# Optimization experiments

Measured on AMD Instinct MI355X. Metric: run time of the kernel, lower is better.

## Reference

```python
import jax, jax.numpy as jnp
import numpy as np
from jax import lax

B, C, H, W = 4, 256, 64, 64
M = 8
CP = C // M  # 32 attention channels
KS = (3, 5, 7, 9)
EPS = 1e-5


def conv1x1(a, w, b):
    # a: [B,Ci,H,W], w: [Co,Ci], b: [Co]
    return jnp.einsum('bchw,oc->bohw', a, w) + b[None, :, None, None]


def _patches(a, k):
    # im2col with padding k//2, stride 1 (matches torch.nn.Unfold(k,1,k//2,1))
    pad = k // 2
    p = lax.conv_general_dilated_patches(a, (k, k), (1, 1), [(pad, pad), (pad, pad)])
    Bb, Cc = a.shape[0], a.shape[1]
    return p.reshape(Bb, Cc, k * k, a.shape[2], a.shape[3])  # [B,C',k^2,H,W]


def local_attn(km, qm, xm, k):
    # query is the center of each patch == qm itself (stride 1, pad k//2)
    kp = _patches(km, k)                                   # [B,C',k^2,H,W]
    scores = jnp.einsum('bckhw,bchw->bkhw', kp, qm)        # per-pixel k^2 logits
    attn = jax.nn.softmax(scores, axis=1)                  # softmax over window (dim=-2 in torch)
    xp = _patches(xm, k)                                   # [B,C',k^2,H,W]
    return jnp.einsum('bckhw,bkhw->bchw', xp, attn)        # [B,C',H,W]


def setup_inputs() -> dict:
    key = jax.random.key(0)
    ks = jax.random.split(key, 12)
    s_in = 1.0 / np.sqrt(C)
    s_out = 1.0 / np.sqrt(CP)
    return {
        'x': jax.random.normal(ks[0], (B, C, H, W), jnp.float32),
        'vessel': jax.random.uniform(ks[1], (B, 1, H, W), jnp.float32),
        'wk': jax.random.normal(ks[2], (CP, C), jnp.float32) * s_in,
        'bk': jnp.zeros((CP,), jnp.float32),
        'wq': jax.random.normal(ks[3], (CP, C), jnp.float32) * s_in,
        'bq': jnp.zeros((CP,), jnp.float32),
        'wx': jax.random.normal(ks[4], (CP, C), jnp.float32) * s_in,
        'bx': jnp.zeros((CP,), jnp.float32),
        'wf': jax.random.normal(ks[5], (C, CP), jnp.float32) * s_out,
        'bf': jnp.zeros((C,), jnp.float32),
        'gamma': jnp.ones((C,), jnp.float32),
        'beta': jnp.zeros((C,), jnp.float32),
    }


def reference(x, vessel, wk, bk, wq, bq, wx, bx, wf, bf, gamma, beta):
    km = conv1x1(x, wk, bk) * vessel   # key map masked by vessel
    qm = conv1x1(x, wq, bq)            # query map
    xm = conv1x1(x, wx, bx)            # value map
    pre = local_attn(km, qm, xm, KS[0])
    for k in KS[1:]:
        pre = pre + local_attn(km, qm, xm, k)
    y = conv1x1(pre, wf, bf)           # [B,C,H,W]
    # BatchNorm2d (training-mode batch stats)
    mean = y.mean(axis=(0, 2, 3), keepdims=True)
    var = y.var(axis=(0, 2, 3), keepdims=True)
    yn = (y - mean) * lax.rsqrt(var + EPS)
    return x + gamma[None, :, None, None] * yn + beta[None, :, None, None]
```

## Files before the change

### kernel.cpp

```cpp
#include <hip/hip_runtime.h>
#include <hip/hip_bf16.h>

typedef __hip_bfloat16 bf16;
typedef unsigned short u16;
typedef unsigned int u32;

typedef __bf16 bf16x8 __attribute__((ext_vector_type(8)));
typedef float f32x4 __attribute__((ext_vector_type(4)));

__device__ __forceinline__ float bf2f(bf16 v) { return __bfloat162float(v); }
__device__ __forceinline__ float us2f(u16 u) {
    union { u32 i; float f; } c; c.i = ((u32)u) << 16; return c.f;
}
__device__ __forceinline__ u16 f2u(float f) {
    union { bf16 b; u16 u; } c; c.b = __float2bfloat16(f); return c.u;
}
__device__ __forceinline__ void up8(const uint4 v, float* f) {
    f[0] = us2f((u16)(v.x & 0xffff)); f[1] = us2f((u16)(v.x >> 16));
    f[2] = us2f((u16)(v.y & 0xffff)); f[3] = us2f((u16)(v.y >> 16));
    f[4] = us2f((u16)(v.z & 0xffff)); f[5] = us2f((u16)(v.z >> 16));
    f[6] = us2f((u16)(v.w & 0xffff)); f[7] = us2f((u16)(v.w >> 16));
}

__global__ __launch_bounds__(256) void k_proj(
    const float* __restrict__ x, const float* __restrict__ vessel,
    const float* __restrict__ wk, const float* __restrict__ bk,
    const float* __restrict__ wq, const float* __restrict__ bq,
    const float* __restrict__ wx, const float* __restrict__ bx,
    bf16* __restrict__ km, bf16* __restrict__ qm, bf16* __restrict__ xm)
{
    __shared__ u16 xs[64 * 264];
    __shared__ u16 wsh[48 * 264];
    const int tid = threadIdx.x;
    const int bid = blockIdx.x;
    const int nh = bid & 1;
    const int pt = bid >> 1;
    const int b  = pt >> 6;
    const int p0 = (pt & 63) * 64;

#pragma unroll
    for (int i = 0; i < 16; ++i) {
        const int idx4 = tid + i * 256;
        const int ch = idx4 >> 4;
        const int px4 = (idx4 & 15) * 4;
        const float4 v = *(const float4*)&x[(b * 256 + ch) * 4096 + p0 + px4];
        xs[(px4 + 0) * 264 + ch] = f2u(v.x);
        xs[(px4 + 1) * 264 + ch] = f2u(v.y);
        xs[(px4 + 2) * 264 + ch] = f2u(v.z);
        xs[(px4 + 3) * 264 + ch] = f2u(v.w);
    }
#pragma unroll
    for (int i = 0; i < 12; ++i) {
        const int idx4 = tid + i * 256;
        const int o = idx4 >> 6;
        const int ch4 = (idx4 & 63) * 4;
        const int go = nh * 48 + o;
        const float* wp = (go < 32) ? wk : ((go < 64) ? wq : wx);
        const float4 v = *(const float4*)&wp[(go & 31) * 256 + ch4];
        wsh[o * 264 + ch4 + 0] = f2u(v.x);
        wsh[o * 264 + ch4 + 1] = f2u(v.y);
        wsh[o * 264 + ch4 + 2] = f2u(v.z);
        wsh[o * 264 + ch4 + 3] = f2u(v.w);
    }
    __syncthreads();

    const int w = tid >> 6;
    const int lane = tid & 63;
    const int lm = lane & 15, quad = lane >> 4;

    f32x4 acc0 = {0.f, 0.f, 0.f, 0.f};
    f32x4 acc1 = {0.f, 0.f, 0.f, 0.f};
    f32x4 acc2 = {0.f, 0.f, 0.f, 0.f};
#pragma unroll
    for (int kk = 0; kk < 8; ++kk) {
        const int k0 = kk * 32 + quad * 8;
        const bf16x8 a  = *(const bf16x8*)&xs[(w * 16 + lm) * 264 + k0];
        const bf16x8 b0 = *(const bf16x8*)&wsh[(0 + lm) * 264 + k0];
        const bf16x8 b1 = *(const bf16x8*)&wsh[(16 + lm) * 264 + k0];
        const bf16x8 b2 = *(const bf16x8*)&wsh[(32 + lm) * 264 + k0];
        acc0 = __builtin_amdgcn_mfma_f32_16x16x32_bf16(a, b0, acc0, 0, 0, 0);
        acc1 = __builtin_amdgcn_mfma_f32_16x16x32_bf16(a, b1, acc1, 0, 0, 0);
        acc2 = __builtin_amdgcn_mfma_f32_16x16x32_bf16(a, b2, acc2, 0, 0, 0);
    }
#pragma unroll
    for (int t = 0; t < 3; ++t) {
        const f32x4 acc = (t == 0) ? acc0 : ((t == 1) ? acc1 : acc2);
        const int go = nh * 48 + t * 16 + lm;
        const float* bs = (go < 32) ? bk : ((go < 64) ? bq : bx);
        const float bias = bs[go & 31];
        bf16* dst = (go < 32) ? km : ((go < 64) ? qm : xm);
#pragma unroll
        for (int rg = 0; rg < 4; ++rg) {
            const int px = p0 + w * 16 + quad * 4 + rg;
            float vv = acc[rg] + bias;
            if (go < 32) vv *= vessel[b * 4096 + px];
            dst[(b * 4096 + px) * 32 + (go & 31)] = __float2bfloat16(vv);
        }
    }
}

__global__ __launch_bounds__(256) void k_attn(
    const bf16* __restrict__ km, const bf16* __restrict__ qm,
    const bf16* __restrict__ xm, bf16* __restrict__ pre)
{
    __shared__ u16 kT[192 * 40];
    __shared__ u16 qs[32 * 40];
    __shared__ u16 xTt[32 * 200];
    __shared__ float S[32 * 196];
    u16* P = kT;

    const int tid = threadIdx.x;
    const int b = blockIdx.x >> 7;
    const int t128 = blockIdx.x & 127;
    const int h0 = (t128 >> 3) * 4;
    const int w0 = (t128 & 7) * 8;
    const u16* uk = (const u16*)km;
    const u16* ux = (const u16*)xm;
    const uint4 z4 = {0u, 0u, 0u, 0u};

#pragma unroll
    for (int i = 0; i < 3; ++i) {
        const int idx4 = tid + i * 256;
        const int pos = idx4 >> 2, c8 = idx4 & 3;
        const int gh = h0 - 4 + (pos >> 4), gw = w0 - 4 + (pos & 15);
        uint4 kv = z4, xv = z4;
        if (gh >= 0 && gh < 64 && gw >= 0 && gw < 64) {
            const int g = ((b << 12) + (gh << 6) + gw) * 32 + c8 * 8;
            kv = *(const uint4*)&uk[g];
            xv = *(const uint4*)&ux[g];
        }
        *(uint4*)&kT[pos * 40 + c8 * 8] = kv;
        const u16* xu = (const u16*)&xv;
#pragma unroll
        for (int t = 0; t < 8; ++t)
            xTt[(c8 * 8 + t) * 200 + pos] = xu[t];
    }
    if (tid < 128) {
        const int px = tid >> 2, c8 = tid & 3;
        const int gh = h0 + (px >> 3), gw = w0 + (px & 7);
        const int g = ((b << 12) + (gh << 6) + gw) * 32 + c8 * 8;
        *(uint4*)&qs[px * 40 + c8 * 8] = *(const uint4*)&((const u16*)qm)[g];
    }
    __syncthreads();

    const int w = tid >> 6;
    const int lane = tid & 63;
    const int lm = lane & 15, quad = lane >> 4;

#pragma unroll
    for (int i = 0; i < 6; ++i) {
        const int t = w + i * 4;
        const int m = t / 12, n = t - m * 12;
        const bf16x8 a = *(const bf16x8*)&qs[(m * 16 + lm) * 40 + quad * 8];
        const bf16x8 bb = *(const bf16x8*)&kT[(n * 16 + lm) * 40 + quad * 8];
        f32x4 acc = {0.f, 0.f, 0.f, 0.f};
        acc = __builtin_amdgcn_mfma_f32_16x16x32_bf16(a, bb, acc, 0, 0, 0);
#pragma unroll
        for (int rg = 0; rg < 4; ++rg)
            S[(m * 16 + quad * 4 + rg) * 196 + n * 16 + lm] = acc[rg];
    }
    __syncthreads();

    const int px = tid >> 3, cg = tid & 7;
    const int ty = px >> 3, tx = px & 7;
    float e[24];
    float Z3 = 0.f, Z5 = 0.f, Z7 = 0.f, Z9 = 0.f;
#pragma unroll
    for (int i = 0; i < 24; ++i) {
        const int pos = cg + 8 * i;
        const int hy = pos >> 4, hx = pos & 15;
        const int dy = hy - 4 - ty, dx = hx - 4 - tx;
        const int ady = dy < 0 ? -dy : dy, adx = dx < 0 ? -dx : dx;
        const int r = ady > adx ? ady : adx;
        const float s = S[px * 196 + pos];
        const float ev = (r <= 4) ? __expf(s) : 0.f;
        e[i] = ev;
        if (r <= 1) Z3 += ev;
        if (r <= 2) Z5 += ev;
        if (r <= 3) Z7 += ev;
        Z9 += ev;
    }
#pragma unroll
    for (int m = 1; m <= 4; m <<= 1) {
        Z3 += __shfl_xor(Z3, m);
        Z5 += __shfl_xor(Z5, m);
        Z7 += __shfl_xor(Z7, m);
        Z9 += __shfl_xor(Z9, m);
    }
    const float iZ3 = 1.f / Z3, iZ5 = 1.f / Z5, iZ7 = 1.f / Z7, iZ9 = 1.f / Z9;
#pragma unroll
    for (int i = 0; i < 24; ++i) {
        const int pos = cg + 8 * i;
        const int hy = pos >> 4, hx = pos & 15;
        const int dy = hy - 4 - ty, dx = hx - 4 - tx;
        const int ady = dy < 0 ? -dy : dy, adx = dx < 0 ? -dx : dx;
        const int r = ady > adx ? ady : adx;
        float coef = iZ9;
        if (r <= 1) coef += iZ3;
        if (r <= 2) coef += iZ5;
        if (r <= 3) coef += iZ7;
        P[px * 200 + pos] = f2u(e[i] * coef);
    }
    __syncthreads();

    const int m0 = w >> 1, n0 = w & 1;
    f32x4 acc = {0.f, 0.f, 0.f, 0.f};
#pragma unroll
    for (int kk = 0; kk < 6; ++kk) {
        const int k0 = kk * 32 + quad * 8;
        const bf16x8 a = *(const bf16x8*)&P[(m0 * 16 + lm) * 200 + k0];
        const bf16x8 bb = *(const bf16x8*)&xTt[(n0 * 16 + lm) * 200 + k0];
        acc = __builtin_amdgcn_mfma_f32_16x16x32_bf16(a, bb, acc, 0, 0, 0);
    }
#pragma unroll
    for (int rg = 0; rg < 4; ++rg) {
        const int pl = m0 * 16 + quad * 4 + rg;
        const int gh = h0 + (pl >> 3), gw = w0 + (pl & 7);
        pre[(((b << 12) + (gh << 6) + gw) << 5) + n0 * 16 + lm] =
            __float2bfloat16(acc[rg]);
    }
}

__global__ __launch_bounds__(256) void k_cov(
    const bf16* __restrict__ pre, float* __restrict__ partials)
{
    __shared__ float t[256 * 32];
    const int tid = threadIdx.x;
    const int p0 = blockIdx.x * 256;
    for (int i = 0; i < 32; ++i) {
        const int idx = tid + i * 256;
        t[idx] = bf2f(pre[p0 * 32 + idx]);
    }
    __syncthreads();
    const int i0 = tid >> 3, j0 = (tid & 7) * 4;
    float4 a = {0.f, 0.f, 0.f, 0.f};
    for (int p = 0; p < 256; ++p) {
        const float vi = t[p * 32 + i0];
        const float4 vj = *(const float4*)&t[p * 32 + j0];
        a.x += vi * vj.x; a.y += vi * vj.y; a.z += vi * vj.z; a.w += vi * vj.w;
    }
    *(float4*)&partials[blockIdx.x * 1056 + i0 * 32 + j0] = a;
    if (tid < 32) {
        float s = 0.f;
        for (int p = 0; p < 256; ++p) s += t[p * 32 + tid];
        partials[blockIdx.x * 1056 + 1024 + tid] = s;
    }
}

__global__ __launch_bounds__(256) void k_stats(
    const float* __restrict__ partials, const float* __restrict__ wf,
    const float* __restrict__ bfb, const float* __restrict__ gamma,
    const float* __restrict__ beta,
    float* __restrict__ Aout, float* __restrict__ Sout)
{
    __shared__ float cov[1024];
    __shared__ float mu[32];
    const int tid = threadIdx.x;
    float4 a = {0.f, 0.f, 0.f, 0.f};
    for (int blk = 0; blk < 64; ++blk) {
        const float4 p = *(const float4*)&partials[blk * 1056 + tid * 4];
        a.x += p.x; a.y += p.y; a.z += p.z; a.w += p.w;
    }
    *(float4*)&cov[tid * 4] = a;
    if (tid < 32) {
        float s = 0.f;
        for (int blk = 0; blk < 64; ++blk) s += partials[blk * 1056 + 1024 + tid];
        mu[tid] = s * (1.f / 16384.f);
    }
    __syncthreads();
    float wo[32];
#pragma unroll
    for (int c = 0; c < 32; ++c) wo[c] = wf[tid * 32 + c];
    float mv = 0.f;
#pragma unroll
    for (int c = 0; c < 32; ++c) mv += wo[c] * mu[c];
    float qacc = 0.f;
    for (int i2 = 0; i2 < 32; ++i2) {
        float t = 0.f;
#pragma unroll
        for (int j2 = 0; j2 < 32; ++j2) t += wo[j2] * cov[i2 * 32 + j2];
        qacc += wo[i2] * t;
    }
    const float var = qacc * (1.f / 16384.f) - mv * mv;
    const float A = gamma[tid] * rsqrtf(var + 1e-5f);
    Aout[tid] = A;
    Sout[tid] = beta[tid] - A * (mv + bfb[tid]);
}

__global__ __launch_bounds__(256) void k_out(
    const bf16* __restrict__ pre, const float* __restrict__ wf,
    const float* __restrict__ bfb, const float* __restrict__ x,
    const float* __restrict__ A, const float* __restrict__ S,
    float* __restrict__ out)
{
    __shared__ float wfL[256 * 32];
    __shared__ float pL[64 * 36];
    const int tid = threadIdx.x;
    const int gp0 = blockIdx.x * 64;
    const int b = gp0 >> 12, p0 = gp0 & 4095;
#pragma unroll
    for (int i = 0; i < 8; ++i) {
        const int idx4 = tid + i * 256;
        *(float4*)&wfL[idx4 * 4] = *(const float4*)&wf[idx4 * 4];
    }
    for (int i = 0; i < 8; ++i) {
        const int idx = tid + i * 256;
        const int p = idx >> 5, c = idx & 31;
        pL[p * 36 + c] = bf2f(pre[gp0 * 32 + idx]);
    }
    __syncthreads();
    const int og = tid >> 6, px = tid & 63;
    float4 pv[8];
#pragma unroll
    for (int c4 = 0; c4 < 8; ++c4)
        pv[c4] = *(const float4*)&pL[px * 36 + c4 * 4];
#pragma unroll
    for (int g = 0; g < 4; ++g) {
        float acc[16];
#pragma unroll
        for (int jj = 0; jj < 16; ++jj) acc[jj] = bfb[og * 64 + g * 16 + jj];
#pragma unroll
        for (int c4 = 0; c4 < 8; ++c4) {
            const float4 xv = pv[c4];
#pragma unroll
            for (int jj = 0; jj < 16; ++jj) {
                const float4 wv = *(const float4*)&wfL[(og * 64 + g * 16 + jj) * 32 + c4 * 4];
                acc[jj] += wv.x * xv.x + wv.y * xv.y + wv.z * xv.z + wv.w * xv.w;
            }
        }
#pragma unroll
        for (int jj = 0; jj < 16; ++jj) {
            const int o = og * 64 + g * 16 + jj;
            const int ga = ((b << 8) + o) * 4096 + p0 + px;
            out[ga] = x[ga] + A[o] * acc[jj] + S[o];
        }
    }
}

extern "C" void kernel_launch(void* const* d_in, const int* in_sizes, int n_in,
                              void* d_out, int out_size, void* d_ws, size_t ws_size,
                              hipStream_t stream)
{
    (void)in_sizes; (void)n_in; (void)out_size; (void)ws_size;
    float* out = (float*)d_out;
    char* ws = (char*)d_ws;

    const float* x      = (const float*)d_in[0];
    const float* vessel = (const float*)d_in[1];
    const float* wk     = (const float*)d_in[2];
    const float* bk     = (const float*)d_in[3];
    const float* wq     = (const float*)d_in[4];
    const float* bq     = (const float*)d_in[5];
    const float* wx     = (const float*)d_in[6];
    const float* bx     = (const float*)d_in[7];
    const float* wf     = (const float*)d_in[8];
    const float* bfb    = (const float*)d_in[9];
    const float* gamma  = (const float*)d_in[10];
    const float* beta   = (const float*)d_in[11];

    bf16* km  = (bf16*)(ws);
    bf16* qm  = (bf16*)(ws + 1048576);
    bf16* xm  = (bf16*)(ws + 2097152);
    bf16* pre = (bf16*)(ws + 3145728);
    float* partials = (float*)(ws + 4194304);
    float* Abuf     = (float*)(ws + 4464640);
    float* Sbuf     = (float*)(ws + 4465664);

    k_proj <<<512, 256, 0, stream>>>(x, vessel, wk, bk, wq, bq, wx, bx,
                                     km, qm, xm);
    k_attn <<<512, 256, 0, stream>>>(km, qm, xm, pre);
    k_cov  <<< 64, 256, 0, stream>>>(pre, partials);
    k_stats<<<  1, 256, 0, stream>>>(partials, wf, bfb, gamma, beta, Abuf, Sbuf);
    k_out  <<<256, 256, 0, stream>>>(pre, wf, bfb, x, Abuf, Sbuf, out);
}
```

Baseline: 135.9 us.

## Fuse covariance into attention kernel and use split-bf16 MFMA for output projection

The covariance/sum reduction is folded into the attention kernel using an MFMA on the per-tile pre values, accumulated with atomics into 64 partial slots that k_proj now zeroes, which removes the separate k_cov launch and its reread of pre. The query tile is read directly from global memory instead of being staged in LDS, and k_attn gets a launch-bounds occupancy hint. The output 1x1 conv becomes an MFMA GEMM with wf split into high and low bf16 parts (prepared in k_stats), over 512 blocks of 32 pixels. The bf bias is dropped because BatchNorm cancels it. The atomics make the float accumulation order nondeterministic.

After: 124.7 us. -8.2%, faster.

```diff
diff --git a/kernel.cpp b/kernel.cpp
--- a/kernel.cpp
+++ b/kernel.cpp
@@ -14,12 +14,6 @@
 }
 __device__ __forceinline__ u16 f2u(float f) {
     union { bf16 b; u16 u; } c; c.b = __float2bfloat16(f); return c.u;
-}
-__device__ __forceinline__ void up8(const uint4 v, float* f) {
-    f[0] = us2f((u16)(v.x & 0xffff)); f[1] = us2f((u16)(v.x >> 16));
-    f[2] = us2f((u16)(v.y & 0xffff)); f[3] = us2f((u16)(v.y >> 16));
-    f[4] = us2f((u16)(v.z & 0xffff)); f[5] = us2f((u16)(v.z >> 16));
-    f[6] = us2f((u16)(v.w & 0xffff)); f[7] = us2f((u16)(v.w >> 16));
 }
 
 __global__ __launch_bounds__(256) void k_proj(
@@ -27,7 +21,8 @@
     const float* __restrict__ wk, const float* __restrict__ bk,
     const float* __restrict__ wq, const float* __restrict__ bq,
     const float* __restrict__ wx, const float* __restrict__ bx,
-    bf16* __restrict__ km, bf16* __restrict__ qm, bf16* __restrict__ xm)
+    bf16* __restrict__ km, bf16* __restrict__ qm, bf16* __restrict__ xm,
+    float* __restrict__ partials)
 {
     __shared__ u16 xs[64 * 264];
     __shared__ u16 wsh[48 * 264];
@@ -37,6 +32,14 @@
     const int pt = bid >> 1;
     const int b  = pt >> 6;
     const int p0 = (pt & 63) * 64;
+
+    if (bid < 64) {
+#pragma unroll
+        for (int i = 0; i < 5; ++i) {
+            const int idx = tid + i * 256;
+            if (idx < 1056) partials[bid * 1056 + idx] = 0.f;
+        }
+    }
 
 #pragma unroll
     for (int i = 0; i < 16; ++i) {
@@ -99,15 +102,16 @@
     }
 }
 
-__global__ __launch_bounds__(256) void k_attn(
+__global__ __launch_bounds__(256, 3) void k_attn(
     const bf16* __restrict__ km, const bf16* __restrict__ qm,
-    const bf16* __restrict__ xm, bf16* __restrict__ pre)
+    const bf16* __restrict__ xm, bf16* __restrict__ pre,
+    float* __restrict__ partials)
 {
     __shared__ u16 kT[192 * 40];
-    __shared__ u16 qs[32 * 40];
     __shared__ u16 xTt[32 * 200];
     __shared__ float S[32 * 196];
     u16* P = kT;
+    u16* preT = (u16*)S;
 
     const int tid = threadIdx.x;
     const int b = blockIdx.x >> 7;
@@ -116,6 +120,7 @@
     const int w0 = (t128 & 7) * 8;
     const u16* uk = (const u16*)km;
     const u16* ux = (const u16*)xm;
+    const u16* uq = (const u16*)qm;
     const uint4 z4 = {0u, 0u, 0u, 0u};
 
 #pragma unroll
@@ -135,12 +140,6 @@
         for (int t = 0; t < 8; ++t)
             xTt[(c8 * 8 + t) * 200 + pos] = xu[t];
     }
-    if (tid < 128) {
-        const int px = tid >> 2, c8 = tid & 3;
-        const int gh = h0 + (px >> 3), gw = w0 + (px & 7);
-        const int g = ((b << 12) + (gh << 6) + gw) * 32 + c8 * 8;
-        *(uint4*)&qs[px * 40 + c8 * 8] = *(const uint4*)&((const u16*)qm)[g];
-    }
     __syncthreads();
 
     const int w = tid >> 6;
@@ -151,7 +150,10 @@
     for (int i = 0; i < 6; ++i) {
         const int t = w + i * 4;
         const int m = t / 12, n = t - m * 12;
-        const bf16x8 a = *(const bf16x8*)&qs[(m * 16 + lm) * 40 + quad * 8];
+        const int am = m * 16 + lm;
+        const int qgh = h0 + (am >> 3), qgw = w0 + (am & 7);
+        const bf16x8 a =
+            *(const bf16x8*)&uq[(((b << 12) + (qgh << 6) + qgw) << 5) + quad * 8];
         const bf16x8 bb = *(const bf16x8*)&kT[(n * 16 + lm) * 40 + quad * 8];
         f32x4 acc = {0.f, 0.f, 0.f, 0.f};
         acc = __builtin_amdgcn_mfma_f32_16x16x32_bf16(a, bb, acc, 0, 0, 0);
@@ -218,40 +220,37 @@
         const int gh = h0 + (pl >> 3), gw = w0 + (pl & 7);
         pre[(((b << 12) + (gh << 6) + gw) << 5) + n0 * 16 + lm] =
             __float2bfloat16(acc[rg]);
-    }
-}
-
-__global__ __launch_bounds__(256) void k_cov(
-    const bf16* __restrict__ pre, float* __restrict__ partials)
-{
-    __shared__ float t[256 * 32];
-    const int tid = threadIdx.x;
-    const int p0 = blockIdx.x * 256;
-    for (int i = 0; i < 32; ++i) {
-        const int idx = tid + i * 256;
-        t[idx] = bf2f(pre[p0 * 32 + idx]);
-    }
-    __syncthreads();
-    const int i0 = tid >> 3, j0 = (tid & 7) * 4;
-    float4 a = {0.f, 0.f, 0.f, 0.f};
-    for (int p = 0; p < 256; ++p) {
-        const float vi = t[p * 32 + i0];
-        const float4 vj = *(const float4*)&t[p * 32 + j0];
-        a.x += vi * vj.x; a.y += vi * vj.y; a.z += vi * vj.z; a.w += vi * vj.w;
-    }
-    *(float4*)&partials[blockIdx.x * 1056 + i0 * 32 + j0] = a;
-    if (tid < 32) {
+        preT[(n0 * 16 + lm) * 40 + pl] = f2u(acc[rg]);
+    }
+    __syncthreads();
+
+    const int it = w >> 1, jt = w & 1;
+    const bf16x8 ca = *(const bf16x8*)&preT[(it * 16 + lm) * 40 + quad * 8];
+    const bf16x8 cb = *(const bf16x8*)&preT[(jt * 16 + lm) * 40 + quad * 8];
+    f32x4 cacc = {0.f, 0.f, 0.f, 0.f};
+    cacc = __builtin_amdgcn_mfma_f32_16x16x32_bf16(ca, cb, cacc, 0, 0, 0);
+    float* pslot = &partials[(blockIdx.x & 63) * 1056];
+#pragma unroll
+    for (int rg = 0; rg < 4; ++rg) {
+        const int ii = it * 16 + quad * 4 + rg, jj = jt * 16 + lm;
+        atomicAdd(&pslot[ii * 32 + jj], cacc[rg]);
+    }
+    if (tid < 128) {
+        const int cc = tid >> 2, sg = tid & 3;
         float s = 0.f;
-        for (int p = 0; p < 256; ++p) s += t[p * 32 + tid];
-        partials[blockIdx.x * 1056 + 1024 + tid] = s;
+#pragma unroll
+        for (int p = 0; p < 8; ++p) s += us2f(preT[cc * 40 + sg * 8 + p]);
+        s += __shfl_xor(s, 1);
+        s += __shfl_xor(s, 2);
+        if (sg == 0) atomicAdd(&pslot[1024 + cc], s);
     }
 }
 
 __global__ __launch_bounds__(256) void k_stats(
     const float* __restrict__ partials, const float* __restrict__ wf,
-    const float* __restrict__ bfb, const float* __restrict__ gamma,
-    const float* __restrict__ beta,
-    float* __restrict__ Aout, float* __restrict__ Sout)
+    const float* __restrict__ gamma, const float* __restrict__ beta,
+    float* __restrict__ Aout, float* __restrict__ Sout,
+    u16* __restrict__ wfh, u16* __restrict__ wfl)
 {
     __shared__ float cov[1024];
     __shared__ float mu[32];
@@ -271,6 +270,22 @@
     float wo[32];
 #pragma unroll
     for (int c = 0; c < 32; ++c) wo[c] = wf[tid * 32 + c];
+
+    __attribute__((aligned(16))) u16 hb[32];
+    __attribute__((aligned(16))) u16 lb[32];
+#pragma unroll
+    for (int c = 0; c < 32; ++c) {
+        const float v = wo[c];
+        const u16 h = f2u(v);
+        hb[c] = h;
+        lb[c] = f2u(v - us2f(h));
+    }
+#pragma unroll
+    for (int c8 = 0; c8 < 4; ++c8) {
+        *(uint4*)&wfh[tid * 32 + c8 * 8] = *(const uint4*)&hb[c8 * 8];
+        *(uint4*)&wfl[tid * 32 + c8 * 8] = *(const uint4*)&lb[c8 * 8];
+    }
+
     float mv = 0.f;
 #pragma unroll
     for (int c = 0; c < 32; ++c) mv += wo[c] * mu[c];
@@ -284,55 +299,70 @@
     const float var = qacc * (1.f / 16384.f) - mv * mv;
     const float A = gamma[tid] * rsqrtf(var + 1e-5f);
     Aout[tid] = A;
-    Sout[tid] = beta[tid] - A * (mv + bfb[tid]);
+    Sout[tid] = beta[tid] - A * mv;
 }
 
 __global__ __launch_bounds__(256) void k_out(
-    const bf16* __restrict__ pre, const float* __restrict__ wf,
-    const float* __restrict__ bfb, const float* __restrict__ x,
+    const bf16* __restrict__ pre, const u16* __restrict__ wfh,
+    const u16* __restrict__ wfl, const float* __restrict__ x,
     const float* __restrict__ A, const float* __restrict__ S,
     float* __restrict__ out)
 {
-    __shared__ float wfL[256 * 32];
-    __shared__ float pL[64 * 36];
+    __shared__ u16 wh[256 * 40];
+    __shared__ u16 wl[256 * 40];
+    __shared__ u16 pL[32 * 40];
     const int tid = threadIdx.x;
-    const int gp0 = blockIdx.x * 64;
+    const int gp0 = blockIdx.x * 32;
     const int b = gp0 >> 12, p0 = gp0 & 4095;
-#pragma unroll
-    for (int i = 0; i < 8; ++i) {
-        const int idx4 = tid + i * 256;
-        *(float4*)&wfL[idx4 * 4] = *(const float4*)&wf[idx4 * 4];
-    }
-    for (int i = 0; i < 8; ++i) {
+
+#pragma unroll
+    for (int i = 0; i < 4; ++i) {
         const int idx = tid + i * 256;
-        const int p = idx >> 5, c = idx & 31;
-        pL[p * 36 + c] = bf2f(pre[gp0 * 32 + idx]);
-    }
-    __syncthreads();
-    const int og = tid >> 6, px = tid & 63;
-    float4 pv[8];
-#pragma unroll
-    for (int c4 = 0; c4 < 8; ++c4)
-        pv[c4] = *(const float4*)&pL[px * 36 + c4 * 4];
-#pragma unroll
-    for (int g = 0; g < 4; ++g) {
-        float acc[16];
-#pragma unroll
-        for (int jj = 0; jj < 16; ++jj) acc[jj] = bfb[og * 64 + g * 16 + jj];
-#pragma unroll
-        for (int c4 = 0; c4 < 8; ++c4) {
-            const float4 xv = pv[c4];
-#pragma unroll
-            for (int jj = 0; jj < 16; ++jj) {
-                const float4 wv = *(const float4*)&wfL[(og * 64 + g * 16 + jj) * 32 + c4 * 4];
-                acc[jj] += wv.x * xv.x + wv.y * xv.y + wv.z * xv.z + wv.w * xv.w;
+        const int o = idx >> 2, c8 = idx & 3;
+        *(uint4*)&wh[o * 40 + c8 * 8] = *(const uint4*)&wfh[o * 32 + c8 * 8];
+        *(uint4*)&wl[o * 40 + c8 * 8] = *(const uint4*)&wfl[o * 32 + c8 * 8];
+    }
+    if (tid < 128) {
+        const int px = tid >> 2, c8 = tid & 3;
+        *(uint4*)&pL[px * 40 + c8 * 8] =
+            *(const uint4*)&((const u16*)pre)[(gp0 + px) * 32 + c8 * 8];
+    }
+    __syncthreads();
+
+    const int w = tid >> 6;
+    const int lane = tid & 63;
+    const int lm = lane & 15, quad = lane >> 4;
+
+    bf16x8 pb[2];
+    pb[0] = *(const bf16x8*)&pL[(0 + lm) * 40 + quad * 8];
+    pb[1] = *(const bf16x8*)&pL[(16 + lm) * 40 + quad * 8];
+
+    f32x4 acc[4][2];
+#pragma unroll
+    for (int mm = 0; mm < 4; ++mm) {
+        const int orow = w * 64 + mm * 16 + lm;
+        const bf16x8 ah = *(const bf16x8*)&wh[orow * 40 + quad * 8];
+        const bf16x8 al = *(const bf16x8*)&wl[orow * 40 + quad * 8];
+#pragma unroll
+        for (int n = 0; n < 2; ++n) {
+            f32x4 t = {0.f, 0.f, 0.f, 0.f};
+            t = __builtin_amdgcn_mfma_f32_16x16x32_bf16(ah, pb[n], t, 0, 0, 0);
+            acc[mm][n] =
+                __builtin_amdgcn_mfma_f32_16x16x32_bf16(al, pb[n], t, 0, 0, 0);
+        }
+    }
+
+#pragma unroll
+    for (int mm = 0; mm < 4; ++mm) {
+#pragma unroll
+        for (int rg = 0; rg < 4; ++rg) {
+            const int o = w * 64 + mm * 16 + quad * 4 + rg;
+            const float Ao = A[o], So = S[o];
+#pragma unroll
+            for (int n = 0; n < 2; ++n) {
+                const int ga = ((b << 8) + o) * 4096 + p0 + n * 16 + lm;
+                out[ga] = x[ga] + Ao * acc[mm][n][rg] + So;
             }
-        }
-#pragma unroll
-        for (int jj = 0; jj < 16; ++jj) {
-            const int o = og * 64 + g * 16 + jj;
-            const int ga = ((b << 8) + o) * 4096 + p0 + px;
-            out[ga] = x[ga] + A[o] * acc[jj] + S[o];
         }
     }
 }
@@ -354,7 +384,6 @@
     const float* wx     = (const float*)d_in[6];
     const float* bx     = (const float*)d_in[7];
     const float* wf     = (const float*)d_in[8];
-    const float* bfb    = (const float*)d_in[9];
     const float* gamma  = (const float*)d_in[10];
     const float* beta   = (const float*)d_in[11];
 
@@ -365,11 +394,13 @@
     float* partials = (float*)(ws + 4194304);
     float* Abuf     = (float*)(ws + 4464640);
     float* Sbuf     = (float*)(ws + 4465664);
+    u16*   wfh      = (u16*)  (ws + 4466688);
+    u16*   wfl      = (u16*)  (ws + 4483072);
 
     k_proj <<<512, 256, 0, stream>>>(x, vessel, wk, bk, wq, bq, wx, bx,
-                                     km, qm, xm);
-    k_attn <<<512, 256, 0, stream>>>(km, qm, xm, pre);
-    k_cov  <<< 64, 256, 0, stream>>>(pre, partials);
-    k_stats<<<  1, 256, 0, stream>>>(partials, wf, bfb, gamma, beta, Abuf, Sbuf);
-    k_out  <<<256, 256, 0, stream>>>(pre, wf, bfb, x, Abuf, Sbuf, out);
-}
+                                     km, qm, xm, partials);
+    k_attn <<<512, 256, 0, stream>>>(km, qm, xm, pre, partials);
+    k_stats<<<  1, 256, 0, stream>>>(partials, wf, gamma, beta, Abuf, Sbuf,
+                                     wfh, wfl);
+    k_out  <<<512, 256, 0, stream>>>(pre, wfh, wfl, x, Abuf, Sbuf, out);
+}
```
